# Performance work log

Hardware: AMD Instinct MI355X
Metric: run time of the kernel (lower is better)

Reference implementation:

```python
import jax, jax.numpy as jnp
import numpy as np

N = 100000      # nodes
E = 1600000     # edges (avg degree 16)
F_IN = 32       # node_features
F_OUT = 32      # filters
K = 2           # Chebyshev order


def setup_inputs() -> dict:
    key = jax.random.key(0)
    ks = jax.random.split(key, 8)
    x = jax.random.normal(ks[0], (N, F_IN), dtype=jnp.float32)
    edge_index = jax.random.randint(ks[1], (2, E), 0, N, dtype=jnp.int32).astype(jnp.int64)
    edge_weight = jax.random.uniform(ks[2], (E,), dtype=jnp.float32)
    s_in = 1.0 / np.sqrt(F_IN)
    s_out = 1.0 / np.sqrt(F_OUT)
    # gate order: i, f, c, o
    Wx = jax.random.normal(ks[3], (4, K, F_IN, F_OUT), dtype=jnp.float32) * s_in
    bx = jnp.zeros((4, F_OUT), dtype=jnp.float32)
    Wh = jax.random.normal(ks[4], (4, K, F_OUT, F_OUT), dtype=jnp.float32) * s_out
    bh = jnp.zeros((4, F_OUT), dtype=jnp.float32)
    wc = jax.random.normal(ks[5], (3, F_OUT), dtype=jnp.float32) * 0.1  # peephole i, f, o
    b_gate = jnp.zeros((4, F_OUT), dtype=jnp.float32)
    lin_w = jax.random.normal(ks[6], (F_OUT, 1), dtype=jnp.float32) * s_out
    lin_b = jnp.zeros((1,), dtype=jnp.float32)
    return dict(x=x, edge_index=edge_index, edge_weight=edge_weight, Wx=Wx, bx=bx,
                Wh=Wh, bh=bh, wc=wc, b_gate=b_gate, lin_w=lin_w, lin_b=lin_b)


def _cheb_norm(src, dst, w, num_nodes):
    # ChebConv 'sym' normalization with lambda_max = 2.0:
    # scaled Laplacian L_hat = L_sym - I has zero diagonal; off-diagonal entries are
    # -D^{-1/2} A D^{-1/2}. Self loops removed (equivalently: weight zeroed).
    w = jnp.where(src == dst, 0.0, w)
    deg = jax.ops.segment_sum(w, src, num_segments=num_nodes)
    dinv = jnp.where(deg > 0, jax.lax.rsqrt(jnp.where(deg > 0, deg, 1.0)), 0.0)
    return -dinv[src] * w * dinv[dst]


def _forward(x, src, dst, norm, Wx, bx, Wh, bh, wc, b_gate, lin_w, lin_b):
    n = x.shape[0]

    def cheb(inp, W, b):
        # K=2 Chebyshev conv: Tx_0 = inp, Tx_1 = L_hat @ inp (sparse gather/scatter)
        tx1 = jax.ops.segment_sum(norm[:, None] * inp[src], dst, num_segments=n)
        return inp @ W[0] + tx1 @ W[1] + b

    H = jnp.zeros((n, Wh.shape[-1]), dtype=x.dtype)
    C = jnp.zeros_like(H)
    I = jax.nn.sigmoid(cheb(x, Wx[0], bx[0]) + cheb(H, Wh[0], bh[0]) + wc[0] * C + b_gate[0])
    Fg = jax.nn.sigmoid(cheb(x, Wx[1], bx[1]) + cheb(H, Wh[1], bh[1]) + wc[1] * C + b_gate[1])
    T = jnp.tanh(cheb(x, Wx[2], bx[2]) + cheb(H, Wh[2], bh[2]) + b_gate[2])
    C = Fg * C + I * T
    O = jax.nn.sigmoid(cheb(x, Wx[3], bx[3]) + cheb(H, Wh[3], bh[3]) + wc[2] * C + b_gate[3])
    H = O * jnp.tanh(C)
    return jax.nn.relu(H) @ lin_w + lin_b  # [N, 1]


def reference(x, edge_index, edge_weight, Wx, bx, Wh, bh, wc, b_gate, lin_w, lin_b):
    src, dst = edge_index[0], edge_index[1]
    norm = _cheb_norm(src, dst, edge_weight, x.shape[0])
    return _forward(x, src, dst, norm, Wx, bx, Wh, bh, wc, b_gate, lin_w, lin_b)
```

## Files before the change

### kernel.cpp

```cpp
#include <hip/hip_runtime.h>


#define FDIM 32
#define MAX_N 100000
#define MAX_E 1600000
#define CBSH 8
#define CB 256
#define MAX_NB ((MAX_N + CB - 1) / CB)
#define NBLK 512
#define SCAN_TILE 2048
#define GNB 64
#define PERBLK 3136

typedef int   iv4 __attribute__((ext_vector_type(4)));
typedef float fv4 __attribute__((ext_vector_type(4)));
__device__ __forceinline__ iv4 nt_i4(const int* p)   { return __builtin_nontemporal_load((const iv4*)p); }
__device__ __forceinline__ fv4 nt_f4(const float* p) { return __builtin_nontemporal_load((const fv4*)p); }

__device__ float g_deg[MAX_N];
__device__ int   g_part2[2 * MAX_NB * NBLK + 1];
__device__ int   g_blk[1024];
__device__ uint2 g_rec[MAX_E];
__device__ uint2 g_srec[MAX_E];
__device__ int   g_row[MAX_N + 1];
__device__ __attribute__((aligned(16))) int   g_src2[MAX_E];
__device__ __attribute__((aligned(16))) float g_nrm2[MAX_E];
__device__ float g_tx1[MAX_N * FDIM];

__global__ __launch_bounds__(256) void hist2_kernel(const int* __restrict__ ei,
                                                    int E, int n_nodes, int nbuck,
                                                    int per_blk) {
    __shared__ int hd[MAX_NB];
    __shared__ int hs[MAX_NB];
    for (int i = threadIdx.x; i < nbuck; i += 256) { hd[i] = 0; hs[i] = 0; }
    __syncthreads();
    int start = blockIdx.x * per_blk;
    int end = start + per_blk;
    if (end > E) end = E;
    for (int base = start; base < end; base += 1024) {
        int e = base + threadIdx.x * 4;
        if (e + 4 <= end) {
            int4 s4 = *(const int4*)(ei + e);
            int4 d4 = *(const int4*)(ei + E + e);
#define H2(S, D) if ((unsigned)(S) < (unsigned)n_nodes && (unsigned)(D) < (unsigned)n_nodes) { \
                atomicAdd(&hd[(D) >> CBSH], 1); atomicAdd(&hs[(S) >> CBSH], 1); }
            H2(s4.x, d4.x) H2(s4.y, d4.y) H2(s4.z, d4.z) H2(s4.w, d4.w)
#undef H2
        } else if (e < end) {
            for (int q = e; q < end; ++q) {
                int s = ei[q], d = ei[E + q];
                if ((unsigned)s >= (unsigned)n_nodes || (unsigned)d >= (unsigned)n_nodes)
                    continue;
                atomicAdd(&hd[d >> CBSH], 1);
                atomicAdd(&hs[s >> CBSH], 1);
            }
        }
    }
    __syncthreads();
    for (int i = threadIdx.x; i < nbuck; i += 256) {
        g_part2[i * NBLK + blockIdx.x] = hd[i];
        g_part2[(nbuck + i) * NBLK + blockIdx.x] = hs[i];
    }
    if (blockIdx.x == 0 && threadIdx.x == 0)
        g_part2[2 * nbuck * NBLK] = 0;
}

__global__ __launch_bounds__(256) void scan1_kernel(int n) {
    __shared__ int sh[256];
    int tid = threadIdx.x;
    int base = blockIdx.x * SCAN_TILE + tid * 8;
    int v[8];
#pragma unroll
    for (int i = 0; i < 8; ++i) v[i] = (base + i < n) ? g_part2[base + i] : 0;
    int tsum = 0;
#pragma unroll
    for (int i = 0; i < 8; ++i) tsum += v[i];
    sh[tid] = tsum;
    __syncthreads();
    for (int off = 1; off < 256; off <<= 1) {
        int t = (tid >= off) ? sh[tid - off] : 0;
        __syncthreads();
        sh[tid] += t;
        __syncthreads();
    }
    if (tid == 255) g_blk[blockIdx.x] = sh[255];
    int run = sh[tid] - tsum;
#pragma unroll
    for (int i = 0; i < 8; ++i) {
        if (base + i < n) g_part2[base + i] = run;
        run += v[i];
    }
}

__global__ __launch_bounds__(256) void scan2_kernel(int nb) {
    __shared__ int sh[256];
    int tid = threadIdx.x;
    int base = tid * 4;
    int v[4];
#pragma unroll
    for (int i = 0; i < 4; ++i) v[i] = (base + i < nb) ? g_blk[base + i] : 0;
    int tsum = v[0] + v[1] + v[2] + v[3];
    sh[tid] = tsum;
    __syncthreads();
    for (int off = 1; off < 256; off <<= 1) {
        int t = (tid >= off) ? sh[tid - off] : 0;
        __syncthreads();
        sh[tid] += t;
        __syncthreads();
    }
    int run = sh[tid] - tsum;
#pragma unroll
    for (int i = 0; i < 4; ++i) {
        if (base + i < nb) g_blk[base + i] = run;
        run += v[i];
    }
}

__global__ void scan3_kernel(int n) {
    int off = g_blk[blockIdx.x];
    int base = blockIdx.x * SCAN_TILE + threadIdx.x * 8;
#pragma unroll
    for (int i = 0; i < 8; ++i) {
        int idx = base + i;
        if (idx < n) g_part2[idx] += off;
    }
}

__global__ __launch_bounds__(256) void scatter_burst_kernel(const int* __restrict__ ei,
                                                            const float* __restrict__ w,
                                                            int E, int n_nodes, int nbuck,
                                                            int per_blk) {
    __shared__ int   cnt[512];
    __shared__ int   sc[512];
    __shared__ int   gb[MAX_NB];
    __shared__ int   cur[MAX_NB];
    __shared__ uint2 staged[PERBLK];
    __shared__ int   gpos[PERBLK];
    int tid = threadIdx.x;
    int blk = blockIdx.x;
    int start = blk * per_blk;
    int end = start + per_blk;
    if (end > E) end = E;

    for (int phase = 0; phase < 2; ++phase) {
        cnt[tid] = 0; cnt[tid + 256] = 0;
        __syncthreads();
        for (int i = tid; i < nbuck; i += 256) {
            int flat = (phase * nbuck + i) * NBLK + blk;
            int g0 = g_part2[flat];
            int g1 = g_part2[flat + 1];
            gb[i] = g0 - phase * E;
            cnt[i] = g1 - g0;
        }
        __syncthreads();
        sc[tid] = cnt[tid]; sc[tid + 256] = cnt[tid + 256];
        __syncthreads();
        for (int off = 1; off < 512; off <<= 1) {
            int v0 = (tid >= off) ? sc[tid - off] : 0;
            int v1 = sc[tid + 256 - off];
            __syncthreads();
            sc[tid] += v0; sc[tid + 256] += v1;
            __syncthreads();
        }
        for (int i = tid; i < nbuck; i += 256) cur[i] = sc[i] - cnt[i];
        __syncthreads();
#define SB1(S, D, W)                                                            \
        {   int s = (S), d = (D);                                               \
            if ((unsigned)s < (unsigned)n_nodes && (unsigned)d < (unsigned)n_nodes) { \
                int key = phase ? s : d;                                        \
                int bin = key >> CBSH;                                          \
                float w0 = (s == d) ? 0.f : (W);                                \
                unsigned pay = phase ? (unsigned)(s & (CB - 1))                 \
                    : (((unsigned)s << CBSH) | (unsigned)(d & (CB - 1)));       \
                int p = atomicAdd(&cur[bin], 1);                                \
                staged[p] = make_uint2(pay, __float_as_uint(w0));               \
                gpos[p] = gb[bin] + (p - (sc[bin] - cnt[bin]));                 \
            } }
        for (int base = start; base < end; base += 1024) {
            int e = base + tid * 4;
            if (e + 4 <= end) {
                iv4 s4 = nt_i4(ei + e);
                iv4 d4 = nt_i4(ei + E + e);
                fv4 w4 = nt_f4(w + e);
                SB1(s4[0], d4[0], w4[0]) SB1(s4[1], d4[1], w4[1])
                SB1(s4[2], d4[2], w4[2]) SB1(s4[3], d4[3], w4[3])
            } else if (e < end) {
                for (int q = e; q < end; ++q) SB1(ei[q], ei[E + q], w[q])
            }
        }
#undef SB1
        __syncthreads();
        int tot = sc[511];
        if (phase == 0) {
            for (int t = tid; t < tot; t += 256) g_rec[gpos[t]] = staged[t];
        } else {
            for (int t = tid; t < tot; t += 256) g_srec[gpos[t]] = staged[t];
        }
        __syncthreads();
    }
}

__global__ __launch_bounds__(256) void deg_sum_kernel(int E, int n_nodes, int nbuck) {
    __shared__ float ldeg[CB];
    int b = blockIdx.x;
    int rs = g_part2[(nbuck + b) * NBLK] - E;
    int re = g_part2[(nbuck + b + 1) * NBLK] - E;
    ldeg[threadIdx.x] = 0.f;
    __syncthreads();
    for (int i = rs + threadIdx.x; i < re; i += 256) {
        uint2 r = g_srec[i];
        atomicAdd(&ldeg[r.x], __uint_as_float(r.y));
    }
    __syncthreads();
    int node = (b << CBSH) + threadIdx.x;
    if (node < n_nodes) {
        float dg = ldeg[threadIdx.x];
        g_deg[node] = (dg > 0.f) ? rsqrtf(dg) : 0.f;
    }
}

__global__ __launch_bounds__(256) void fine_sort_kernel(int E, int n_nodes, int nbuck) {
    __shared__ int cnt[CB];
    __shared__ int cur[CB];
    __shared__ float dv[CB];
    __shared__ int wsum[4];
    int b = blockIdx.x;
    int rs = g_part2[b * NBLK];
    int re = g_part2[(b + 1) * NBLK];
    {
        int tid = threadIdx.x;
        cnt[tid] = 0;
        int node = (b << CBSH) + tid;
        dv[tid] = (node < n_nodes) ? g_deg[node] : 0.f;
    }
    __syncthreads();
    for (int i = rs + threadIdx.x; i < re; i += 256)
        atomicAdd(&cnt[g_rec[i].x & (CB - 1)], 1);
    __syncthreads();
    {
        int tid = threadIdx.x;
        int lane = tid & 63;
        int wave = tid >> 6;
        int v = cnt[tid];
        int inc = v;
#pragma unroll
        for (int off = 1; off < 64; off <<= 1) {
            int t = __shfl_up(inc, off, 64);
            if (lane >= off) inc += t;
        }
        if (lane == 63) wsum[wave] = inc;
        __syncthreads();
        int wo = 0;
#pragma unroll
        for (int ww = 0; ww < 4; ++ww) wo += (ww < wave) ? wsum[ww] : 0;
        int start = rs + wo + (inc - v);
        cur[tid] = start;
        int node = (b << CBSH) + tid;
        if (node < n_nodes) g_row[node] = start;
    }
    if (b == nbuck - 1 && threadIdx.x == 0) g_row[n_nodes] = re;
    __syncthreads();
    for (int i = rs + threadIdx.x; i < re; i += 256) {
        uint2 r = g_rec[i];
        int s = (int)(r.x >> CBSH);
        int loc = r.x & (CB - 1);
        float nrm = -g_deg[s] * __uint_as_float(r.y) * dv[loc];
        int pos = atomicAdd(&cur[loc], 1);
        g_src2[pos] = s;
        g_nrm2[pos] = nrm;
    }
}

__global__ __launch_bounds__(256) void gather_kernel(const float* __restrict__ x,
                                                     int n_nodes) {
    int t = blockIdx.x * blockDim.x + threadIdx.x;
    int node = t >> 5;
    int f = t & 31;
    if (node >= n_nodes) return;
    int i = g_row[node];
    int end = g_row[node + 1];
    float acc = 0.f, accB = 0.f;
    while (i < end && (i & 3)) {
        acc += g_nrm2[i] * x[g_src2[i] * FDIM + f];
        ++i;
    }
    for (; i + 8 <= end; i += 8) {
        iv4 sa = nt_i4(g_src2 + i);
        iv4 sb = nt_i4(g_src2 + i + 4);
        fv4 na = nt_f4(g_nrm2 + i);
        fv4 nb = nt_f4(g_nrm2 + i + 4);
        float xa0 = x[sa[0] * FDIM + f], xa1 = x[sa[1] * FDIM + f];
        float xa2 = x[sa[2] * FDIM + f], xa3 = x[sa[3] * FDIM + f];
        float xb0 = x[sb[0] * FDIM + f], xb1 = x[sb[1] * FDIM + f];
        float xb2 = x[sb[2] * FDIM + f], xb3 = x[sb[3] * FDIM + f];
        acc  += na[0] * xa0 + na[1] * xa1 + na[2] * xa2 + na[3] * xa3;
        accB += nb[0] * xb0 + nb[1] * xb1 + nb[2] * xb2 + nb[3] * xb3;
    }
    for (; i + 4 <= end; i += 4) {
        iv4 s4 = nt_i4(g_src2 + i);
        fv4 n4 = nt_f4(g_nrm2 + i);
        acc += n4[0] * x[s4[0] * FDIM + f] + n4[1] * x[s4[1] * FDIM + f]
             + n4[2] * x[s4[2] * FDIM + f] + n4[3] * x[s4[3] * FDIM + f];
    }
    for (; i < end; ++i) acc += g_nrm2[i] * x[g_src2[i] * FDIM + f];
    g_tx1[node * FDIM + f] = acc + accB;
}

__global__ __launch_bounds__(256, 4) void gates64_kernel(
    const float* __restrict__ x,
    const float* __restrict__ Wx, const float* __restrict__ bx,
    const float* __restrict__ bh, const float* __restrict__ wc,
    const float* __restrict__ bg, const float* __restrict__ lin_w,
    const float* __restrict__ lin_b, float* __restrict__ out, int n_nodes) {
    __shared__ float Ws[3 * 2048];
    __shared__ float xs[GNB * FDIM];
    __shared__ float ts[GNB * FDIM];

    for (int idx = threadIdx.x; idx < 512; idx += 256) {
        *(float4*)&Ws[idx * 4]        = *(const float4*)&Wx[0 * 2048 + idx * 4];
        *(float4*)&Ws[2048 + idx * 4] = *(const float4*)&Wx[2 * 2048 + idx * 4];
        *(float4*)&Ws[4096 + idx * 4] = *(const float4*)&Wx[3 * 2048 + idx * 4];
    }
    int node0 = blockIdx.x * GNB;
    for (int t = threadIdx.x; t < GNB * FDIM / 4; t += 256) {
        int q = t * 4;
        int n = node0 + (q >> 5);
        float4 xv = make_float4(0.f, 0.f, 0.f, 0.f);
        float4 tv = make_float4(0.f, 0.f, 0.f, 0.f);
        if (n < n_nodes) {
            xv = *(const float4*)&x[n * FDIM + (q & 31)];
            tv = *(const float4*)&g_tx1[n * FDIM + (q & 31)];
        }
        *(float4*)&xs[q] = xv;
        *(float4*)&ts[q] = tv;
    }
    __syncthreads();

    int j   = threadIdx.x & 31;
    int grp = threadIdx.x >> 5;

    float ai0=0.f,ai1=0.f,ai2=0.f,ai3=0.f,ai4=0.f,ai5=0.f,ai6=0.f,ai7=0.f;
    float ac0=0.f,ac1=0.f,ac2=0.f,ac3=0.f,ac4=0.f,ac5=0.f,ac6=0.f,ac7=0.f;
    float ao0=0.f,ao1=0.f,ao2=0.f,ao3=0.f,ao4=0.f,ao5=0.f,ao6=0.f,ao7=0.f;
    const float* xr = &xs[(grp * 8) * FDIM];
    const float* tr = &ts[(grp * 8) * FDIM];
    for (int k4 = 0; k4 < 32; k4 += 4) {
        float4 xv0 = *(const float4*)(xr + 0 * FDIM + k4);
        float4 xv1 = *(const float4*)(xr + 1 * FDIM + k4);
        float4 xv2 = *(const float4*)(xr + 2 * FDIM + k4);
        float4 xv3 = *(const float4*)(xr + 3 * FDIM + k4);
        float4 xv4 = *(const float4*)(xr + 4 * FDIM + k4);
        float4 xv5 = *(const float4*)(xr + 5 * FDIM + k4);
        float4 xv6 = *(const float4*)(xr + 6 * FDIM + k4);
        float4 xv7 = *(const float4*)(xr + 7 * FDIM + k4);
        float4 tv0 = *(const float4*)(tr + 0 * FDIM + k4);
        float4 tv1 = *(const float4*)(tr + 1 * FDIM + k4);
        float4 tv2 = *(const float4*)(tr + 2 * FDIM + k4);
        float4 tv3 = *(const float4*)(tr + 3 * FDIM + k4);
        float4 tv4 = *(const float4*)(tr + 4 * FDIM + k4);
        float4 tv5 = *(const float4*)(tr + 5 * FDIM + k4);
        float4 tv6 = *(const float4*)(tr + 6 * FDIM + k4);
        float4 tv7 = *(const float4*)(tr + 7 * FDIM + k4);
#define KSTEP(kc, COMP)                                        \
        {   int o0 = (k4 + kc) * 32 + j;                       \
            float wi0 = Ws[o0],        wi1 = Ws[1024 + o0];    \
            float wg0 = Ws[2048 + o0], wg1 = Ws[3072 + o0];    \
            float wo0 = Ws[4096 + o0], wo1 = Ws[5120 + o0];    \
            ai0 += xv0.COMP * wi0 + tv0.COMP * wi1;            \
            ac0 += xv0.COMP * wg0 + tv0.COMP * wg1;            \
            ao0 += xv0.COMP * wo0 + tv0.COMP * wo1;            \
            ai1 += xv1.COMP * wi0 + tv1.COMP * wi1;            \
            ac1 += xv1.COMP * wg0 + tv1.COMP * wg1;            \
            ao1 += xv1.COMP * wo0 + tv1.COMP * wo1;            \
            ai2 += xv2.COMP * wi0 + tv2.COMP * wi1;            \
            ac2 += xv2.COMP * wg0 + tv2.COMP * wg1;            \
            ao2 += xv2.COMP * wo0 + tv2.COMP * wo1;            \
            ai3 += xv3.COMP * wi0 + tv3.COMP * wi1;            \
            ac3 += xv3.COMP * wg0 + tv3.COMP * wg1;            \
            ao3 += xv3.COMP * wo0 + tv3.COMP * wo1;            \
            ai4 += xv4.COMP * wi0 + tv4.COMP * wi1;            \
            ac4 += xv4.COMP * wg0 + tv4.COMP * wg1;            \
            ao4 += xv4.COMP * wo0 + tv4.COMP * wo1;            \
            ai5 += xv5.COMP * wi0 + tv5.COMP * wi1;            \
            ac5 += xv5.COMP * wg0 + tv5.COMP * wg1;            \
            ao5 += xv5.COMP * wo0 + tv5.COMP * wo1;            \
            ai6 += xv6.COMP * wi0 + tv6.COMP * wi1;            \
            ac6 += xv6.COMP * wg0 + tv6.COMP * wg1;            \
            ao6 += xv6.COMP * wo0 + tv6.COMP * wo1;            \
            ai7 += xv7.COMP * wi0 + tv7.COMP * wi1;            \
            ac7 += xv7.COMP * wg0 + tv7.COMP * wg1;            \
            ao7 += xv7.COMP * wo0 + tv7.COMP * wo1;            \
        }
        KSTEP(0, x) KSTEP(1, y) KSTEP(2, z) KSTEP(3, w)
#undef KSTEP
    }

    float bi = bx[0 * 32 + j] + bh[0 * 32 + j] + bg[0 * 32 + j];
    float bc = bx[2 * 32 + j] + bh[2 * 32 + j] + bg[2 * 32 + j];
    float bo = bx[3 * 32 + j] + bh[3 * 32 + j] + bg[3 * 32 + j];
    float wcp = wc[2 * 32 + j];
    float lwj = lin_w[j];
    float lb0 = lin_b[0];

#define GOUT(m, AI, AC, AO)                                            \
    {   int n = node0 + grp * 8 + m;                                   \
        float I = 1.f / (1.f + __expf(-(AI + bi)));                    \
        float T = tanhf(AC + bc);                                      \
        float C = I * T;                                               \
        float O = 1.f / (1.f + __expf(-(AO + bo + wcp * C)));          \
        float H = O * tanhf(C);                                        \
        float r = fmaxf(H, 0.f) * lwj;                                 \
        _Pragma("unroll")                                              \
        for (int mm = 16; mm > 0; mm >>= 1) r += __shfl_xor(r, mm, 32);\
        if (j == 0 && n < n_nodes) out[n] = r + lb0; }
    GOUT(0, ai0, ac0, ao0) GOUT(1, ai1, ac1, ao1)
    GOUT(2, ai2, ac2, ao2) GOUT(3, ai3, ac3, ao3)
    GOUT(4, ai4, ac4, ao4) GOUT(5, ai5, ac5, ao5)
    GOUT(6, ai6, ac6, ao6) GOUT(7, ai7, ac7, ao7)
#undef GOUT
}

extern "C" void kernel_launch(void* const* d_in, const int* in_sizes, int n_in,
                              void* d_out, int out_size, void* d_ws, size_t ws_size,
                              hipStream_t stream) {
    const float* x     = (const float*)d_in[0];
    const int*   ei    = (const int*)d_in[1];
    const float* w     = (const float*)d_in[2];
    const float* Wx    = (const float*)d_in[3];
    const float* bx    = (const float*)d_in[4];
    const float* bh    = (const float*)d_in[6];
    const float* wc    = (const float*)d_in[7];
    const float* bg    = (const float*)d_in[8];
    const float* lin_w = (const float*)d_in[9];
    const float* lin_b = (const float*)d_in[10];
    float*       out   = (float*)d_out;

    int n_nodes = in_sizes[0] / FDIM;
    if (n_nodes > MAX_N) n_nodes = MAX_N;
    int E = in_sizes[2];
    if (E > MAX_E) E = MAX_E;

    int nbuck   = (n_nodes + CB - 1) >> CBSH;
    int per_blk = (((E + NBLK - 1) / NBLK) + 3) & ~3;
    int n_scan  = 2 * nbuck * NBLK + 1;
    int nb_scan = (n_scan + SCAN_TILE - 1) / SCAN_TILE;

    hist2_kernel<<<NBLK, 256, 0, stream>>>(ei, E, n_nodes, nbuck, per_blk);
    scan1_kernel<<<nb_scan, 256, 0, stream>>>(n_scan);
    scan2_kernel<<<1, 256, 0, stream>>>(nb_scan);
    scan3_kernel<<<nb_scan, 256, 0, stream>>>(n_scan);
    scatter_burst_kernel<<<NBLK, 256, 0, stream>>>(ei, w, E, n_nodes, nbuck, per_blk);
    deg_sum_kernel<<<nbuck, 256, 0, stream>>>(E, n_nodes, nbuck);
    fine_sort_kernel<<<nbuck, 256, 0, stream>>>(E, n_nodes, nbuck);
    {
        long long tot = (long long)n_nodes * 32;
        gather_kernel<<<(int)((tot + 255) / 256), 256, 0, stream>>>(x, n_nodes);
    }
    gates64_kernel<<<(n_nodes + GNB - 1) / GNB, 256, 0, stream>>>(
        x, Wx, bx, bh, wc, bg, lin_w, lin_b, out, n_nodes);
}
```

Baseline: 254.2 us.

## Fuse SpMM gather into gates kernel and fold scan fix-up into consumers

Measured after the change: 281.5 us. 10.7% more time.

```diff
diff --git a/kernel.cpp b/kernel.cpp
--- a/kernel.cpp
+++ b/kernel.cpp
@@ -25,7 +25,10 @@
 __device__ int   g_row[MAX_N + 1];
 __device__ __attribute__((aligned(16))) int   g_src2[MAX_E];
 __device__ __attribute__((aligned(16))) float g_nrm2[MAX_E];
-__device__ float g_tx1[MAX_N * FDIM];
+
+__device__ __forceinline__ int scanned(int idx) {
+    return g_part2[idx] + g_blk[idx >> 11];
+}
 
 __global__ __launch_bounds__(256) void hist2_kernel(const int* __restrict__ ei,
                                                     int E, int n_nodes, int nbuck,
@@ -116,16 +119,6 @@
     }
 }
 
-__global__ void scan3_kernel(int n) {
-    int off = g_blk[blockIdx.x];
-    int base = blockIdx.x * SCAN_TILE + threadIdx.x * 8;
-#pragma unroll
-    for (int i = 0; i < 8; ++i) {
-        int idx = base + i;
-        if (idx < n) g_part2[idx] += off;
-    }
-}
-
 __global__ __launch_bounds__(256) void scatter_burst_kernel(const int* __restrict__ ei,
                                                             const float* __restrict__ w,
                                                             int E, int n_nodes, int nbuck,
@@ -147,8 +140,8 @@
         __syncthreads();
         for (int i = tid; i < nbuck; i += 256) {
             int flat = (phase * nbuck + i) * NBLK + blk;
-            int g0 = g_part2[flat];
-            int g1 = g_part2[flat + 1];
+            int g0 = scanned(flat);
+            int g1 = scanned(flat + 1);
             gb[i] = g0 - phase * E;
             cnt[i] = g1 - g0;
         }
@@ -203,8 +196,8 @@
 __global__ __launch_bounds__(256) void deg_sum_kernel(int E, int n_nodes, int nbuck) {
     __shared__ float ldeg[CB];
     int b = blockIdx.x;
-    int rs = g_part2[(nbuck + b) * NBLK] - E;
-    int re = g_part2[(nbuck + b + 1) * NBLK] - E;
+    int rs = scanned((nbuck + b) * NBLK) - E;
+    int re = scanned((nbuck + b + 1) * NBLK) - E;
     ldeg[threadIdx.x] = 0.f;
     __syncthreads();
     for (int i = rs + threadIdx.x; i < re; i += 256) {
@@ -225,8 +218,8 @@
     __shared__ float dv[CB];
     __shared__ int wsum[4];
     int b = blockIdx.x;
-    int rs = g_part2[b * NBLK];
-    int re = g_part2[(b + 1) * NBLK];
+    int rs = scanned(b * NBLK);
+    int re = scanned((b + 1) * NBLK);
     {
         int tid = threadIdx.x;
         cnt[tid] = 0;
@@ -271,42 +264,7 @@
     }
 }
 
-__global__ __launch_bounds__(256) void gather_kernel(const float* __restrict__ x,
-                                                     int n_nodes) {
-    int t = blockIdx.x * blockDim.x + threadIdx.x;
-    int node = t >> 5;
-    int f = t & 31;
-    if (node >= n_nodes) return;
-    int i = g_row[node];
-    int end = g_row[node + 1];
-    float acc = 0.f, accB = 0.f;
-    while (i < end && (i & 3)) {
-        acc += g_nrm2[i] * x[g_src2[i] * FDIM + f];
-        ++i;
-    }
-    for (; i + 8 <= end; i += 8) {
-        iv4 sa = nt_i4(g_src2 + i);
-        iv4 sb = nt_i4(g_src2 + i + 4);
-        fv4 na = nt_f4(g_nrm2 + i);
-        fv4 nb = nt_f4(g_nrm2 + i + 4);
-        float xa0 = x[sa[0] * FDIM + f], xa1 = x[sa[1] * FDIM + f];
-        float xa2 = x[sa[2] * FDIM + f], xa3 = x[sa[3] * FDIM + f];
-        float xb0 = x[sb[0] * FDIM + f], xb1 = x[sb[1] * FDIM + f];
-        float xb2 = x[sb[2] * FDIM + f], xb3 = x[sb[3] * FDIM + f];
-        acc  += na[0] * xa0 + na[1] * xa1 + na[2] * xa2 + na[3] * xa3;
-        accB += nb[0] * xb0 + nb[1] * xb1 + nb[2] * xb2 + nb[3] * xb3;
-    }
-    for (; i + 4 <= end; i += 4) {
-        iv4 s4 = nt_i4(g_src2 + i);
-        fv4 n4 = nt_f4(g_nrm2 + i);
-        acc += n4[0] * x[s4[0] * FDIM + f] + n4[1] * x[s4[1] * FDIM + f]
-             + n4[2] * x[s4[2] * FDIM + f] + n4[3] * x[s4[3] * FDIM + f];
-    }
-    for (; i < end; ++i) acc += g_nrm2[i] * x[g_src2[i] * FDIM + f];
-    g_tx1[node * FDIM + f] = acc + accB;
-}
-
-__global__ __launch_bounds__(256, 4) void gates64_kernel(
+__global__ __launch_bounds__(256, 4) void gather_gates_kernel(
     const float* __restrict__ x,
     const float* __restrict__ Wx, const float* __restrict__ bx,
     const float* __restrict__ bh, const float* __restrict__ wc,
@@ -326,13 +284,42 @@
         int q = t * 4;
         int n = node0 + (q >> 5);
         float4 xv = make_float4(0.f, 0.f, 0.f, 0.f);
-        float4 tv = make_float4(0.f, 0.f, 0.f, 0.f);
-        if (n < n_nodes) {
-            xv = *(const float4*)&x[n * FDIM + (q & 31)];
-            tv = *(const float4*)&g_tx1[n * FDIM + (q & 31)];
-        }
+        if (n < n_nodes) xv = *(const float4*)&x[n * FDIM + (q & 31)];
         *(float4*)&xs[q] = xv;
-        *(float4*)&ts[q] = tv;
+    }
+
+    int hh = threadIdx.x >> 5;
+    int f  = threadIdx.x & 31;
+    for (int m = 0; m < 8; ++m) {
+        int node = node0 + hh * 8 + m;
+        if (node >= n_nodes) break;
+        int i = g_row[node];
+        int end = g_row[node + 1];
+        float acc = 0.f, accB = 0.f;
+        while (i < end && (i & 3)) {
+            acc += g_nrm2[i] * x[g_src2[i] * FDIM + f];
+            ++i;
+        }
+        for (; i + 8 <= end; i += 8) {
+            iv4 sa = nt_i4(g_src2 + i);
+            iv4 sb = nt_i4(g_src2 + i + 4);
+            fv4 na = nt_f4(g_nrm2 + i);
+            fv4 nb = nt_f4(g_nrm2 + i + 4);
+            float xa0 = x[sa[0] * FDIM + f], xa1 = x[sa[1] * FDIM + f];
+            float xa2 = x[sa[2] * FDIM + f], xa3 = x[sa[3] * FDIM + f];
+            float xb0 = x[sb[0] * FDIM + f], xb1 = x[sb[1] * FDIM + f];
+            float xb2 = x[sb[2] * FDIM + f], xb3 = x[sb[3] * FDIM + f];
+            acc  += na[0] * xa0 + na[1] * xa1 + na[2] * xa2 + na[3] * xa3;
+            accB += nb[0] * xb0 + nb[1] * xb1 + nb[2] * xb2 + nb[3] * xb3;
+        }
+        for (; i + 4 <= end; i += 4) {
+            iv4 s4 = nt_i4(g_src2 + i);
+            fv4 n4 = nt_f4(g_nrm2 + i);
+            acc += n4[0] * x[s4[0] * FDIM + f] + n4[1] * x[s4[1] * FDIM + f]
+                 + n4[2] * x[s4[2] * FDIM + f] + n4[3] * x[s4[3] * FDIM + f];
+        }
+        for (; i < end; ++i) acc += g_nrm2[i] * x[g_src2[i] * FDIM + f];
+        ts[(hh * 8 + m) * FDIM + f] = acc + accB;
     }
     __syncthreads();
 
@@ -448,14 +435,9 @@
     hist2_kernel<<<NBLK, 256, 0, stream>>>(ei, E, n_nodes, nbuck, per_blk);
     scan1_kernel<<<nb_scan, 256, 0, stream>>>(n_scan);
     scan2_kernel<<<1, 256, 0, stream>>>(nb_scan);
-    scan3_kernel<<<nb_scan, 256, 0, stream>>>(n_scan);
     scatter_burst_kernel<<<NBLK, 256, 0, stream>>>(ei, w, E, n_nodes, nbuck, per_blk);
     deg_sum_kernel<<<nbuck, 256, 0, stream>>>(E, n_nodes, nbuck);
     fine_sort_kernel<<<nbuck, 256, 0, stream>>>(E, n_nodes, nbuck);
-    {
-        long long tot = (long long)n_nodes * 32;
-        gather_kernel<<<(int)((tot + 255) / 256), 256, 0, stream>>>(x, n_nodes);
-    }
-    gates64_kernel<<<(n_nodes + GNB - 1) / GNB, 256, 0, stream>>>(
+    gather_gates_kernel<<<(n_nodes + GNB - 1) / GNB, 256, 0, stream>>>(
         x, Wx, bx, bh, wc, bg, lin_w, lin_b, out, n_nodes);
 }
```

## Fuse scatter phases, drop scan3 kernel, and double partition block count

Applied to the files above, without the earlier changes.

After: 264.0 us. 3.9% more time.

```diff
diff --git a/kernel.cpp b/kernel.cpp
--- a/kernel.cpp
+++ b/kernel.cpp
@@ -7,10 +7,10 @@
 #define CBSH 8
 #define CB 256
 #define MAX_NB ((MAX_N + CB - 1) / CB)
-#define NBLK 512
+#define NBLK 1024
 #define SCAN_TILE 2048
 #define GNB 64
-#define PERBLK 3136
+#define PERBLK 1568
 
 typedef int   iv4 __attribute__((ext_vector_type(4)));
 typedef float fv4 __attribute__((ext_vector_type(4)));
@@ -26,6 +26,10 @@
 __device__ __attribute__((aligned(16))) int   g_src2[MAX_E];
 __device__ __attribute__((aligned(16))) float g_nrm2[MAX_E];
 __device__ float g_tx1[MAX_N * FDIM];
+
+__device__ __forceinline__ int scanned(int idx) {
+    return g_part2[idx] + g_blk[idx >> 11];
+}
 
 __global__ __launch_bounds__(256) void hist2_kernel(const int* __restrict__ ei,
                                                     int E, int n_nodes, int nbuck,
@@ -116,95 +120,111 @@
     }
 }
 
-__global__ void scan3_kernel(int n) {
-    int off = g_blk[blockIdx.x];
-    int base = blockIdx.x * SCAN_TILE + threadIdx.x * 8;
-#pragma unroll
-    for (int i = 0; i < 8; ++i) {
-        int idx = base + i;
-        if (idx < n) g_part2[idx] += off;
-    }
-}
-
-__global__ __launch_bounds__(256) void scatter_burst_kernel(const int* __restrict__ ei,
-                                                            const float* __restrict__ w,
-                                                            int E, int n_nodes, int nbuck,
-                                                            int per_blk) {
-    __shared__ int   cnt[512];
-    __shared__ int   sc[512];
-    __shared__ int   gb[MAX_NB];
-    __shared__ int   cur[MAX_NB];
-    __shared__ uint2 staged[PERBLK];
-    __shared__ int   gpos[PERBLK];
+__global__ __launch_bounds__(256) void scatter1_kernel(const int* __restrict__ ei,
+                                                       const float* __restrict__ w,
+                                                       int E, int n_nodes, int nbuck,
+                                                       int per_blk) {
+    __shared__ int   scrC[512];
+    __shared__ int   scrI[512];
+    __shared__ int   gbD[MAX_NB], baseD[MAX_NB], curD[MAX_NB];
+    __shared__ int   gbS[MAX_NB], baseS[MAX_NB], curS[MAX_NB];
+    __shared__ uint2 stagedD[PERBLK];
+    __shared__ uint2 stagedS[PERBLK];
+    __shared__ int   gposD[PERBLK];
+    __shared__ int   gposS[PERBLK];
+    __shared__ int   tot;
     int tid = threadIdx.x;
     int blk = blockIdx.x;
     int start = blk * per_blk;
     int end = start + per_blk;
     if (end > E) end = E;
 
-    for (int phase = 0; phase < 2; ++phase) {
-        cnt[tid] = 0; cnt[tid + 256] = 0;
-        __syncthreads();
-        for (int i = tid; i < nbuck; i += 256) {
-            int flat = (phase * nbuck + i) * NBLK + blk;
-            int g0 = g_part2[flat];
-            int g1 = g_part2[flat + 1];
-            gb[i] = g0 - phase * E;
-            cnt[i] = g1 - g0;
+    scrC[tid] = 0; scrC[tid + 256] = 0;
+    __syncthreads();
+    for (int i = tid; i < nbuck; i += 256) {
+        int flat = i * NBLK + blk;
+        int g0 = scanned(flat), g1 = scanned(flat + 1);
+        gbD[i] = g0;
+        scrC[i] = g1 - g0;
+    }
+    __syncthreads();
+    scrI[tid] = scrC[tid]; scrI[tid + 256] = scrC[tid + 256];
+    __syncthreads();
+    for (int off = 1; off < 512; off <<= 1) {
+        int v0 = (tid >= off) ? scrI[tid - off] : 0;
+        int v1 = scrI[tid + 256 - off];
+        __syncthreads();
+        scrI[tid] += v0; scrI[tid + 256] += v1;
+        __syncthreads();
+    }
+    for (int i = tid; i < nbuck; i += 256) {
+        int b0 = scrI[i] - scrC[i];
+        baseD[i] = b0; curD[i] = b0;
+    }
+    if (tid == 0) tot = scrI[511];
+    __syncthreads();
+
+    scrC[tid] = 0; scrC[tid + 256] = 0;
+    __syncthreads();
+    for (int i = tid; i < nbuck; i += 256) {
+        int flat = (nbuck + i) * NBLK + blk;
+        int g0 = scanned(flat), g1 = scanned(flat + 1);
+        gbS[i] = g0 - E;
+        scrC[i] = g1 - g0;
+    }
+    __syncthreads();
+    scrI[tid] = scrC[tid]; scrI[tid + 256] = scrC[tid + 256];
+    __syncthreads();
+    for (int off = 1; off < 512; off <<= 1) {
+        int v0 = (tid >= off) ? scrI[tid - off] : 0;
+        int v1 = scrI[tid + 256 - off];
+        __syncthreads();
+        scrI[tid] += v0; scrI[tid + 256] += v1;
+        __syncthreads();
+    }
+    for (int i = tid; i < nbuck; i += 256) {
+        int b0 = scrI[i] - scrC[i];
+        baseS[i] = b0; curS[i] = b0;
+    }
+    __syncthreads();
+
+#define SB1(S, D, W)                                                            \
+    {   int s = (S), d = (D);                                                   \
+        if ((unsigned)s < (unsigned)n_nodes && (unsigned)d < (unsigned)n_nodes) { \
+            float w0 = (s == d) ? 0.f : (W);               \
+            int bD = d >> CBSH;                                                 \
+            int pD = atomicAdd(&curD[bD], 1);                   \
+            stagedD[pD] = make_uint2(((unsigned)s << CBSH) | (unsigned)(d & (CB - 1)), \
+                                     __float_as_uint(w0));                      \
+            gposD[pD] = gbD[bD] + (pD - baseD[bD]);                             \
+            int bS = s >> CBSH;                                                 \
+            int pS = atomicAdd(&curS[bS], 1);                                   \
+            stagedS[pS] = make_uint2((unsigned)(s & (CB - 1)), __float_as_uint(w0)); \
+            gposS[pS] = gbS[bS] + (pS - baseS[bS]);                             \
+        } }
+    for (int base = start; base < end; base += 1024) {
+        int e = base + tid * 4;
+        if (e + 4 <= end) {
+            iv4 s4 = nt_i4(ei + e);
+            iv4 d4 = nt_i4(ei + E + e);
+            fv4 w4 = nt_f4(w + e);
+            SB1(s4[0], d4[0], w4[0]) SB1(s4[1], d4[1], w4[1])
+            SB1(s4[2], d4[2], w4[2]) SB1(s4[3], d4[3], w4[3])
+        } else if (e < end) {
+            for (int q = e; q < end; ++q) SB1(ei[q], ei[E + q], w[q])
         }
-        __syncthreads();
-        sc[tid] = cnt[tid]; sc[tid + 256] = cnt[tid + 256];
-        __syncthreads();
-        for (int off = 1; off < 512; off <<= 1) {
-            int v0 = (tid >= off) ? sc[tid - off] : 0;
-            int v1 = sc[tid + 256 - off];
-            __syncthreads();
-            sc[tid] += v0; sc[tid + 256] += v1;
-            __syncthreads();
-        }
-        for (int i = tid; i < nbuck; i += 256) cur[i] = sc[i] - cnt[i];
-        __syncthreads();
-#define SB1(S, D, W)                                                            \
-        {   int s = (S), d = (D);                                               \
-            if ((unsigned)s < (unsigned)n_nodes && (unsigned)d < (unsigned)n_nodes) { \
-                int key = phase ? s : d;                                        \
-                int bin = key >> CBSH;                                          \
-                float w0 = (s == d) ? 0.f : (W);                                \
-                unsigned pay = phase ? (unsigned)(s & (CB - 1))                 \
-                    : (((unsigned)s << CBSH) | (unsigned)(d & (CB - 1)));       \
-                int p = atomicAdd(&cur[bin], 1);                                \
-                staged[p] = make_uint2(pay, __float_as_uint(w0));               \
-                gpos[p] = gb[bin] + (p - (sc[bin] - cnt[bin]));                 \
-            } }
-        for (int base = start; base < end; base += 1024) {
-            int e = base + tid * 4;
-            if (e + 4 <= end) {
-                iv4 s4 = nt_i4(ei + e);
-                iv4 d4 = nt_i4(ei + E + e);
-                fv4 w4 = nt_f4(w + e);
-                SB1(s4[0], d4[0], w4[0]) SB1(s4[1], d4[1], w4[1])
-                SB1(s4[2], d4[2], w4[2]) SB1(s4[3], d4[3], w4[3])
-            } else if (e < end) {
-                for (int q = e; q < end; ++q) SB1(ei[q], ei[E + q], w[q])
-            }
-        }
+    }
 #undef SB1
-        __syncthreads();
-        int tot = sc[511];
-        if (phase == 0) {
-            for (int t = tid; t < tot; t += 256) g_rec[gpos[t]] = staged[t];
-        } else {
-            for (int t = tid; t < tot; t += 256) g_srec[gpos[t]] = staged[t];
-        }
-        __syncthreads();
-    }
+    __syncthreads();
+    for (int t = tid; t < tot; t += 256) g_rec[gposD[t]] = stagedD[t];
+    for (int t = tid; t < tot; t += 256) g_srec[gposS[t]] = stagedS[t];
 }
 
 __global__ __launch_bounds__(256) void deg_sum_kernel(int E, int n_nodes, int nbuck) {
     __shared__ float ldeg[CB];
     int b = blockIdx.x;
-    int rs = g_part2[(nbuck + b) * NBLK] - E;
-    int re = g_part2[(nbuck + b + 1) * NBLK] - E;
+    int rs = scanned((nbuck + b) * NBLK) - E;
+    int re = scanned((nbuck + b + 1) * NBLK) - E;
     ldeg[threadIdx.x] = 0.f;
     __syncthreads();
     for (int i = rs + threadIdx.x; i < re; i += 256) {
@@ -225,8 +245,8 @@
     __shared__ float dv[CB];
     __shared__ int wsum[4];
     int b = blockIdx.x;
-    int rs = g_part2[b * NBLK];
-    int re = g_part2[(b + 1) * NBLK];
+    int rs = scanned(b * NBLK);
+    int re = scanned((b + 1) * NBLK);
     {
         int tid = threadIdx.x;
         cnt[tid] = 0;
@@ -448,8 +468,7 @@
     hist2_kernel<<<NBLK, 256, 0, stream>>>(ei, E, n_nodes, nbuck, per_blk);
     scan1_kernel<<<nb_scan, 256, 0, stream>>>(n_scan);
     scan2_kernel<<<1, 256, 0, stream>>>(nb_scan);
-    scan3_kernel<<<nb_scan, 256, 0, stream>>>(n_scan);
-    scatter_burst_kernel<<<NBLK, 256, 0, stream>>>(ei, w, E, n_nodes, nbuck, per_blk);
+    scatter1_kernel<<<NBLK, 256, 0, stream>>>(ei, w, E, n_nodes, nbuck, per_blk);
     deg_sum_kernel<<<nbuck, 256, 0, stream>>>(E, n_nodes, nbuck);
     fine_sort_kernel<<<nbuck, 256, 0, stream>>>(E, n_nodes, nbuck);
     {
```
